# Kernel tuning notes

Hardware: AMD Instinct MI355X
Metric: run time of the kernel (lower is better)

Reference implementation:

```python
import jax, jax.numpy as jnp
import numpy as np

N_GRAPHS = 50
EPS = 1e-5
N_NODES, N_EDGES, F, L, N_HEADS = 50000, 800000, 64, 3, 3


def _bn(x, gamma, beta):
    # BatchNorm1d over nodes, training-mode (biased batch statistics)
    m = x.mean(axis=0)
    v = jnp.mean((x - m) ** 2, axis=0)
    return gamma * (x - m) * jax.lax.rsqrt(v + EPS) + beta


def _pna_layer(x, src, dst, preW, preb, postW, postb, linW, linb, avg_log, avg_lin):
    N = x.shape[0]
    # pre-MLP on concatenated (target x_i, source x_j): [E, 2F] -> [E, F]
    h = jnp.concatenate([x[dst], x[src]], axis=-1) @ preW + preb
    ones = jnp.ones((h.shape[0],), h.dtype)
    cnt = jax.ops.segment_sum(ones, dst, num_segments=N)[:, None]
    has = cnt > 0
    deg = jnp.maximum(cnt, 1.0)  # PNAConv clamps degree to >= 1
    mean = jax.ops.segment_sum(h, dst, num_segments=N) / deg
    mean2 = jax.ops.segment_sum(h * h, dst, num_segments=N) / deg
    std = jnp.sqrt(jax.nn.relu(mean2 - mean * mean) + EPS)
    mn = jnp.where(has, jax.ops.segment_min(h, dst, num_segments=N), 0.0)
    mx = jnp.where(has, jax.ops.segment_max(h, dst, num_segments=N), 0.0)
    aggr = jnp.concatenate([mean, mn, mx, std], axis=-1)  # [N, 4F]
    log_deg = jnp.log(deg + 1.0)
    out = jnp.concatenate([aggr,
                           aggr * (log_deg / avg_log),   # amplification
                           aggr * (avg_log / log_deg),   # attenuation
                           aggr * (deg / avg_lin)],      # linear
                          axis=-1)                       # [N, 16F]
    out = jnp.concatenate([x, out], axis=-1) @ postW + postb  # post-MLP [N, F]
    return out @ linW + linb


def _forward(x, deg_hist, preW, preb, postW, postb, linW, linb, bn_g, bn_b,
             sharedW, sharedb, hW1, hb1, hW2, hb2, hW3, hb3, src, dst, batch):
    bins = jnp.arange(deg_hist.shape[0], dtype=deg_hist.dtype)
    tot = deg_hist.sum()
    avg_lin = (bins * deg_hist).sum() / tot
    avg_log = (jnp.log(bins + 1.0) * deg_hist).sum() / tot
    for l in range(preW.shape[0]):  # only num_conv_layers convs run (zip truncation)
        x = _pna_layer(x, src, dst, preW[l], preb[l], postW[l], postb[l],
                       linW[l], linb[l], avg_log, avg_lin)
        x = jax.nn.relu(_bn(x, bn_g[l], bn_b[l]))
    gcnt = jax.ops.segment_sum(jnp.ones((x.shape[0],), x.dtype), batch,
                               num_segments=N_GRAPHS)[:, None]
    g = jax.ops.segment_sum(x, batch, num_segments=N_GRAPHS) / jnp.maximum(gcnt, 1.0)
    g = jax.nn.relu(g @ sharedW + sharedb)  # shared MLP (num_shared=1)
    h1 = jax.nn.relu(jnp.einsum('gd,hdk->hgk', g, hW1) + hb1[:, None, :])
    h2 = jax.nn.relu(jnp.einsum('hgk,hkm->hgm', h1, hW2) + hb2[:, None, :])
    o = jnp.einsum('hgm,hmo->hgo', h2, hW3) + hb3[:, None, :]  # [H, G, 1]
    return jnp.transpose(o[..., 0])  # [G, H] == torch.cat(head outputs, dim=1)


def setup_inputs():
    key = jax.random.key(0)
    ks = jax.random.split(key, 12)

    def w(k, shape, fan_in):
        return jax.random.normal(k, shape, jnp.float32) / np.sqrt(fan_in)

    return {
        "x": jax.random.normal(ks[0], (N_NODES, F), jnp.float32),
        "edge_index": jax.random.randint(ks[1], (2, N_EDGES), 0, N_NODES),
        "batch": jnp.sort(jax.random.randint(ks[2], (N_NODES,), 0, N_GRAPHS)),
        "deg_hist": jax.random.uniform(ks[3], (33,), jnp.float32) + 0.01,
        "preW": w(ks[4], (L, 2 * F, F), 2 * F),
        "preb": jnp.zeros((L, F), jnp.float32),
        "postW": w(ks[5], (L, 17 * F, F), 17 * F),
        "postb": jnp.zeros((L, F), jnp.float32),
        "linW": w(ks[6], (L, F, F), F),
        "linb": jnp.zeros((L, F), jnp.float32),
        "bn_g": jnp.ones((L, F), jnp.float32),
        "bn_b": jnp.zeros((L, F), jnp.float32),
        "sharedW": w(ks[7], (F, F), F),
        "sharedb": jnp.zeros((F,), jnp.float32),
        "hW1": w(ks[8], (N_HEADS, F, 50), F),
        "hb1": jnp.zeros((N_HEADS, 50), jnp.float32),
        "hW2": w(ks[9], (N_HEADS, 50, 25), 50),
        "hb2": jnp.zeros((N_HEADS, 25), jnp.float32),
        "hW3": w(ks[10], (N_HEADS, 25, 1), 25),
        "hb3": jnp.zeros((N_HEADS, 1), jnp.float32),
    }


def reference(x, edge_index, batch, deg_hist, preW, preb, postW, postb,
              linW, linb, bn_g, bn_b, sharedW, sharedb,
              hW1, hb1, hW2, hb2, hW3, hb3):
    return _forward(x, deg_hist, preW, preb, postW, postb, linW, linb,
                    bn_g, bn_b, sharedW, sharedb, hW1, hb1, hW2, hb2,
                    hW3, hb3, edge_index[0], edge_index[1], batch)
```

## Files before the change

kernel.cpp:

```cpp
#include <hip/hip_runtime.h>
#include <math.h>

#define N_NODES 50000
#define N_EDGES 800000
#define NGRAPHS 50
#define NHEADS 3
#define EPS 1e-5f
#define NWIN 196
#define WSH 8

typedef _Float16 half8 __attribute__((ext_vector_type(8)));
typedef _Float16 half2v __attribute__((ext_vector_type(2)));
typedef float f32x4 __attribute__((ext_vector_type(4)));

__device__ inline half2v h2_shfl_xor(half2v v, int m) {
  int xi = __shfl_xor(*(int*)&v, m, 64);
  return *(half2v*)&xi;
}

__global__ void __launch_bounds__(256) k_zero_setup(int* cnt, float* gsum, float* gcnt,
                                                    float* part, float* partq,
                                                    const float* dh, int nbins, float* scal) {
  int gid = blockIdx.x * 256 + threadIdx.x;
  int gs = gridDim.x * 256;
  for (int i = gid; i < N_NODES; i += gs) cnt[i] = 0;
  for (int i = gid; i < NGRAPHS * 64; i += gs) gsum[i] = 0.f;
  for (int i = gid; i < NGRAPHS; i += gs) gcnt[i] = 0.f;
  for (int i = gid; i < 128 * 64; i += gs) { part[i] = 0.f; partq[i] = 0.f; }
  if (blockIdx.x == 0 && threadIdx.x < 64) {
    int t = threadIdx.x;
    float v = (t < nbins) ? dh[t] : 0.f;
    float lv = logf((float)t + 1.f) * v;
    float bv = (float)t * v;
    for (int d = 32; d > 0; d >>= 1) {
      v  += __shfl_down(v,  d, 64);
      lv += __shfl_down(lv, d, 64);
      bv += __shfl_down(bv, d, 64);
    }
    if (t == 0) { scal[0] = lv / v; scal[1] = bv / v; }
  }
}

__global__ void __launch_bounds__(256) k_hist(const int* __restrict__ dst, int* __restrict__ cnt) {
  int e = blockIdx.x * 256 + threadIdx.x;
  if (e < N_EDGES) atomicAdd(&cnt[dst[e]], 1);
}

__global__ void __launch_bounds__(256) k_scan_a(const int* __restrict__ cnt, int* __restrict__ off,
                                                int* __restrict__ blksum) {
  __shared__ int lds[256];
  int t = threadIdx.x;
  int base = blockIdx.x * 1024 + t * 4;
  int v0 = (base + 0 < N_NODES) ? cnt[base + 0] : 0;
  int v1 = (base + 1 < N_NODES) ? cnt[base + 1] : 0;
  int v2 = (base + 2 < N_NODES) ? cnt[base + 2] : 0;
  int v3 = (base + 3 < N_NODES) ? cnt[base + 3] : 0;
  int tsum = v0 + v1 + v2 + v3;
  lds[t] = tsum; __syncthreads();
  for (int d = 1; d < 256; d <<= 1) {
    int x = (t >= d) ? lds[t - d] : 0;
    __syncthreads();
    lds[t] += x;
    __syncthreads();
  }
  int run = lds[t] - tsum;
  if (base + 0 < N_NODES) off[base + 0] = run; run += v0;
  if (base + 1 < N_NODES) off[base + 1] = run; run += v1;
  if (base + 2 < N_NODES) off[base + 2] = run; run += v2;
  if (base + 3 < N_NODES) off[base + 3] = run;
  if (t == 255) blksum[blockIdx.x] = lds[255];
}

__global__ void __launch_bounds__(64) k_scan_b(const int* __restrict__ blksum, int* __restrict__ blkoff) {
  int t = threadIdx.x;
  int own = (t < 49) ? blksum[t] : 0;
  int v = own;
  for (int d = 1; d < 64; d <<= 1) {
    int u = __shfl_up(v, d, 64);
    if (t >= d) v += u;
  }
  if (t < 49) blkoff[t] = v - own;
}

__global__ void __launch_bounds__(256) k_scan_c(int* __restrict__ off, const int* __restrict__ blkoff,
                                                int* __restrict__ wincur) {
  int i = blockIdx.x * 256 + threadIdx.x;
  if (i < N_NODES) {
    int fo = off[i] + blkoff[i >> 10];
    off[i] = fo;
    if ((i & 255) == 0) wincur[i >> WSH] = fo;
  }
  if (i == 0) off[N_NODES] = N_EDGES;
}

__global__ void __launch_bounds__(256) k_part1(const int* __restrict__ src, const int* __restrict__ dst,
                                               int* __restrict__ wincur, int* __restrict__ pairS,
                                               unsigned char* __restrict__ pairDL) {
  __shared__ int hist[256];
  __shared__ int scan[256];
  __shared__ int baseg[256];
  __shared__ int place[256];
  __shared__ int sS[2048];
  __shared__ unsigned char sDL[2048];
  __shared__ unsigned char sW[2048];
  int t = threadIdx.x;
  int base = blockIdx.x * 2048;
  hist[t] = 0;
  __syncthreads();
  int d[8], s[8];
  #pragma unroll
  for (int i = 0; i < 8; ++i) {
    int e = base + t + 256 * i;
    bool val = e < N_EDGES;
    d[i] = val ? dst[e] : -1;
    s[i] = val ? src[e] : 0;
    if (val) atomicAdd(&hist[d[i] >> WSH], 1);
  }
  __syncthreads();
  int v = hist[t];
  scan[t] = v; __syncthreads();
  for (int dd = 1; dd < 256; dd <<= 1) {
    int x = (t >= dd) ? scan[t - dd] : 0;
    __syncthreads();
    scan[t] += x;
    __syncthreads();
  }
  place[t] = scan[t] - v;
  if (v > 0) baseg[t] = atomicAdd(&wincur[t], v);
  __syncthreads();
  #pragma unroll
  for (int i = 0; i < 8; ++i) {
    if (d[i] >= 0) {
      int w = d[i] >> WSH;
      int p = atomicAdd(&place[w], 1);
      sS[p] = s[i] << 6;
      sDL[p] = (unsigned char)(d[i] & 255);
      sW[p] = (unsigned char)w;
    }
  }
  __syncthreads();
  int tot = min(N_EDGES - base, 2048);
  for (int i = t; i < tot; i += 256) {
    int w = sW[i];
    int gidx = baseg[w] + (i - (scan[w] - hist[w]));
    pairS[gidx] = sS[i];
    pairDL[gidx] = sDL[i];
  }
}

__global__ void __launch_bounds__(256) k_part2(const int* __restrict__ off, const int* __restrict__ pairS,
                                               const unsigned char* __restrict__ pairDL,
                                               int* __restrict__ esrc) {
  __shared__ int curW[256];
  __shared__ int offW[257];
  __shared__ int esrcW[6144];
  int w = blockIdx.x, t = threadIdx.x;
  int n0 = w << WSH;
  offW[t] = off[min(n0 + t, N_NODES)];
  if (t == 0) offW[256] = off[min(n0 + 256, N_NODES)];
  curW[t] = 0;
  __syncthreads();
  int start = offW[0];
  int end = offW[256];
  int cnt = end - start;
  if (cnt <= 6144) {
    for (int i = t; i < cnt; i += 256) {
      int s = pairS[start + i];
      int dl = pairDL[start + i];
      int pos = offW[dl] - start + atomicAdd(&curW[dl], 1);
      esrcW[pos] = s;
    }
    __syncthreads();
    for (int i = t; i < cnt; i += 256) esrc[start + i] = esrcW[i];
  } else {
    for (int i = t; i < cnt; i += 256) {
      int s = pairS[start + i];
      int dl = pairDL[start + i];
      int pos = offW[dl] + atomicAdd(&curW[dl], 1);
      esrc[pos] = s;
    }
  }
}

__global__ void __launch_bounds__(256) k_prep(const float* __restrict__ xin, _Float16* __restrict__ xout,
                                              const float* __restrict__ preW, const float* __restrict__ postW,
                                              const float* __restrict__ linW, _Float16* __restrict__ preP,
                                              _Float16* __restrict__ postAP, _Float16* __restrict__ postBP,
                                              _Float16* __restrict__ linP) {
  int t0 = blockIdx.x * 256 + threadIdx.x;
  if (t0 < 400000) {
    const float* s = xin + (size_t)t0 * 8;
    float4 v0 = *(const float4*)s;
    float4 v1 = *(const float4*)(s + 4);
    half8 h = {(_Float16)v0.x, (_Float16)v0.y, (_Float16)v0.z, (_Float16)v0.w,
               (_Float16)v1.x, (_Float16)v1.y, (_Float16)v1.z, (_Float16)v1.w};
    *(half8*)(xout + (size_t)t0 * 8) = h;
    return;
  }
  int t = t0 - 400000;
  if (t < 24576) {
    int l = t >> 13, r = t & 8191;
    int j = r & 7, lane = (r >> 3) & 63, ctg = (r >> 9) & 7, kc = r >> 12;
    int k = kc * 32 + ((lane >> 4) << 3) + j;
    int col = ctg * 16 + (lane & 15);
    const float* W = preW + (size_t)l * 8192;
    float v = (col < 64) ? W[k * 64 + col] : W[(64 + k) * 64 + (col - 64)];
    preP[(size_t)l * 8192 + r] = (_Float16)v;
  } else if (t < 221184) {
    int q = t - 24576;
    int l = q >> 16, r = q & 65535;
    int j = r & 7, lane = (r >> 3) & 63, ct = (r >> 9) & 3, s = (r >> 11) & 3, kc = r >> 13;
    int kp = kc * 32 + ((lane >> 4) << 3) + j;
    int half = kp >> 7, sec = (kp >> 5) & 3, f = kp & 31;
    int korig = sec * 64 + half * 32 + f;
    int col = ct * 16 + (lane & 15);
    postAP[(size_t)l * 65536 + r] = (_Float16)postW[(size_t)l * 69632 + (size_t)(64 + s * 256 + korig) * 64 + col];
  } else if (t < 233472) {
    int q = t - 221184;
    int l = q >> 12, r = q & 4095;
    int j = r & 7, lane = (r >> 3) & 63, ct = (r >> 9) & 3, kc = r >> 11;
    int k = kc * 32 + ((lane >> 4) << 3) + j;
    int col = ct * 16 + (lane & 15);
    postBP[(size_t)l * 4096 + r] = (_Float16)postW[(size_t)l * 69632 + (size_t)k * 64 + col];
  } else if (t < 245760) {
    int q = t - 233472;
    int l = q >> 12, r = q & 4095;
    int j = r & 7, lane = (r >> 3) & 63, ct = (r >> 9) & 3, kc = r >> 11;
    int k = kc * 32 + ((lane >> 4) << 3) + j;
    int col = ct * 16 + (lane & 15);
    linP[(size_t)l * 4096 + r] = (_Float16)linW[(size_t)l * 4096 + (size_t)k * 64 + col];
  }
}

__global__ void __launch_bounds__(256) k_mfma_g1(const _Float16* __restrict__ yin, const float* __restrict__ bnsc,
                                                 const float* __restrict__ bnsh, int applyBN,
                                                 const _Float16* __restrict__ wp, const float* __restrict__ bias,
                                                 _Float16* __restrict__ Aout, _Float16* __restrict__ B0,
                                                 _Float16* __restrict__ B1, _Float16* __restrict__ xout) {
  int t = threadIdx.x, lane = t & 63, wave = t >> 6;
  int r0 = blockIdx.x * 64;
  int mrow = lane & 15, q8 = ((lane >> 4) << 3);
  f32x4 acc[4][2];
  #pragma unroll
  for (int rt = 0; rt < 4; ++rt) { acc[rt][0] = (f32x4)0.f; acc[rt][1] = (f32x4)0.f; }
  #pragma unroll
  for (int kc = 0; kc < 2; ++kc) {
    int k0 = kc * 32 + q8;
    half8 a[4];
    #pragma unroll
    for (int rt = 0; rt < 4; ++rt) {
      int r = min(r0 + rt * 16 + mrow, N_NODES - 1);
      a[rt] = *(const half8*)(yin + (size_t)r * 64 + k0);
    }
    if (applyBN) {
      float4 sc0 = *(const float4*)(bnsc + k0);
      float4 sc1 = *(const float4*)(bnsc + k0 + 4);
      float4 sh0 = *(const float4*)(bnsh + k0);
      float4 sh1 = *(const float4*)(bnsh + k0 + 4);
      #pragma unroll
      for (int rt = 0; rt < 4; ++rt) {
        half8 v = a[rt];
        v[0] = (_Float16)fmaxf((float)v[0] * sc0.x + sh0.x, 0.f);
        v[1] = (_Float16)fmaxf((float)v[1] * sc0.y + sh0.y, 0.f);
        v[2] = (_Float16)fmaxf((float)v[2] * sc0.z + sh0.z, 0.f);
        v[3] = (_Float16)fmaxf((float)v[3] * sc0.w + sh0.w, 0.f);
        v[4] = (_Float16)fmaxf((float)v[4] * sc1.x + sh1.x, 0.f);
        v[5] = (_Float16)fmaxf((float)v[5] * sc1.y + sh1.y, 0.f);
        v[6] = (_Float16)fmaxf((float)v[6] * sc1.z + sh1.z, 0.f);
        v[7] = (_Float16)fmaxf((float)v[7] * sc1.w + sh1.w, 0.f);
        a[rt] = v;
      }
      if (wave == 0) {
        #pragma unroll
        for (int rt = 0; rt < 4; ++rt) {
          int r = min(r0 + rt * 16 + mrow, N_NODES - 1);
          *(half8*)(xout + (size_t)r * 64 + k0) = a[rt];
        }
      }
    }
    #pragma unroll
    for (int ci = 0; ci < 2; ++ci) {
      int ctg = wave * 2 + ci;
      half8 b = *(const half8*)(wp + (size_t)((kc * 8 + ctg) * 64 + lane) * 8);
      #pragma unroll
      for (int rt = 0; rt < 4; ++rt)
        acc[rt][ci] = __builtin_amdgcn_mfma_f32_16x16x32_f16(a[rt], b, acc[rt][ci], 0, 0, 0);
    }
  }
  #pragma unroll
  for (int ci = 0; ci < 2; ++ci) {
    int col = (wave * 2 + ci) * 16 + mrow;
    float bv = (col < 64) ? bias[col] : 0.f;
    _Float16* outp;
    int stride;
    if (col < 64)      { outp = Aout + col;       stride = 64; }
    else if (col < 96) { outp = B0 + (col - 64);  stride = 32; }
    else               { outp = B1 + (col - 96);  stride = 32; }
    #pragma unroll
    for (int rt = 0; rt < 4; ++rt)
      #pragma unroll
      for (int reg = 0; reg < 4; ++reg) {
        int row = r0 + rt * 16 + ((lane >> 4) << 2) + reg;
        if (row < N_NODES) outp[(size_t)row * stride] = (_Float16)(acc[rt][ci][reg] + bv);
      }
  }
}

__global__ void __launch_bounds__(256) k_aggr(const _Float16* __restrict__ A, const _Float16* __restrict__ B0,
                                              const _Float16* __restrict__ B1, const int* __restrict__ off,
                                              const int* __restrict__ esrc, const float* __restrict__ scal,
                                              _Float16* __restrict__ aggr0, _Float16* __restrict__ aggr1,
                                              float4* __restrict__ scales) {
  int wave = threadIdx.x >> 6, lane = threadIdx.x & 63;
  int b = blockIdx.x;
  int half = (b >> 2) & 1;
  int idx = (b >> 3) * 4 + (b & 3);
  int n = idx * 4 + wave;
  int lh4 = lane & 15, eg = lane >> 4;
  half2v c2 = *(const half2v*)(A + (size_t)n * 64 + half * 32 + lh4 * 2);
  int e0 = __builtin_amdgcn_readfirstlane(off[n]);
  int e1 = __builtin_amdgcn_readfirstlane(off[n + 1]);
  int deg = e1 - e0;
  const char* Bb = (const char*)(half ? B1 : B0);
  int lo4 = lh4 * 4;
  const _Float16 HMAX = (_Float16)65504.f;
  half2v s2 = {(_Float16)0.f, (_Float16)0.f};
  half2v q2 = s2;
  half2v mn2 = {HMAX, HMAX};
  half2v mx2 = {-HMAX, -HMAX};
  int e = e0;
  for (; e + 7 < e1; e += 8) {
    int ra = __builtin_nontemporal_load(esrc + e + eg);
    int rb = __builtin_nontemporal_load(esrc + e + 4 + eg);
    half2v ba = *(const half2v*)(Bb + ra + lo4);
    half2v bb = *(const half2v*)(Bb + rb + lo4);
    s2 += ba; s2 += bb;
    q2 += ba * ba; q2 += bb * bb;
    mn2 = __builtin_elementwise_min(mn2, __builtin_elementwise_min(ba, bb));
    mx2 = __builtin_elementwise_max(mx2, __builtin_elementwise_max(ba, bb));
  }
  for (; e < e1; e += 4) {
    if (e + eg < e1) {
      int r = __builtin_nontemporal_load(esrc + e + eg);
      half2v bv = *(const half2v*)(Bb + r + lo4);
      s2 += bv;
      q2 += bv * bv;
      mn2 = __builtin_elementwise_min(mn2, bv);
      mx2 = __builtin_elementwise_max(mx2, bv);
    }
  }
  s2 += h2_shfl_xor(s2, 16); s2 += h2_shfl_xor(s2, 32);
  q2 += h2_shfl_xor(q2, 16); q2 += h2_shfl_xor(q2, 32);
  mn2 = __builtin_elementwise_min(mn2, h2_shfl_xor(mn2, 16));
  mn2 = __builtin_elementwise_min(mn2, h2_shfl_xor(mn2, 32));
  mx2 = __builtin_elementwise_max(mx2, h2_shfl_xor(mx2, 16));
  mx2 = __builtin_elementwise_max(mx2, h2_shfl_xor(mx2, 32));
  if (eg == 0) {
    _Float16* arow = (half ? aggr1 : aggr0) + (size_t)n * 128;
    half2v w;
    if (deg == 0) {
      w[0] = (_Float16)0.f; w[1] = (_Float16)0.f;
      *(half2v*)(arow + lh4 * 2) = w;
      *(half2v*)(arow + 32 + lh4 * 2) = w;
      *(half2v*)(arow + 64 + lh4 * 2) = w;
      w[0] = (_Float16)sqrtf(EPS); w[1] = w[0];
      *(half2v*)(arow + 96 + lh4 * 2) = w;
    } else {
      float c0 = (float)c2[0], c1 = (float)c2[1];
      float inv = 1.f / (float)deg;
      float mb0 = (float)s2[0] * inv, mb1 = (float)s2[1] * inv;
      float v0 = fmaxf((float)q2[0] * inv - mb0 * mb0, 0.f);
      float v1 = fmaxf((float)q2[1] * inv - mb1 * mb1, 0.f);
      w[0] = (_Float16)(c0 + mb0); w[1] = (_Float16)(c1 + mb1);
      *(half2v*)(arow + lh4 * 2) = w;
      w[0] = (_Float16)(c0 + (float)mn2[0]); w[1] = (_Float16)(c1 + (float)mn2[1]);
      *(half2v*)(arow + 32 + lh4 * 2) = w;
      w[0] = (_Float16)(c0 + (float)mx2[0]); w[1] = (_Float16)(c1 + (float)mx2[1]);
      *(half2v*)(arow + 64 + lh4 * 2) = w;
      w[0] = (_Float16)sqrtf(v0 + EPS); w[1] = (_Float16)sqrtf(v1 + EPS);
      *(half2v*)(arow + 96 + lh4 * 2) = w;
    }
    if (half == 0 && lane == 0) {
      float degf = fmaxf((float)deg, 1.f);
      float ld = logf(degf + 1.f);
      float al = scal[0], av = scal[1];
      scales[n] = make_float4(ld / al, al / ld, degf / av, 0.f);
    }
  }
}

__global__ void __launch_bounds__(256) k_mfma_g23(const _Float16* __restrict__ aggr0, const _Float16* __restrict__ aggr1,
                                                  const _Float16* __restrict__ x16,
                                                  const _Float16* __restrict__ wpA, const _Float16* __restrict__ wpB,
                                                  const float* __restrict__ postb, const float4* __restrict__ scales,
                                                  const _Float16* __restrict__ linP, const float* __restrict__ linb,
                                                  _Float16* __restrict__ y16,
                                                  float* __restrict__ part, float* __restrict__ partq) {
  __shared__ _Float16 yS[64][72];
  int t = threadIdx.x, lane = t & 63, ct = t >> 6;
  int r0 = blockIdx.x * 64;
  int mrow = lane & 15, q8 = ((lane >> 4) << 3);
  f32x4 acc[4][4];
  #pragma unroll
  for (int rt = 0; rt < 4; ++rt)
    #pragma unroll
    for (int s = 0; s < 4; ++s) acc[rt][s] = (f32x4)0.f;
  #pragma unroll 2
  for (int kc = 0; kc < 8; ++kc) {
    const _Float16* ab = (kc < 4) ? aggr0 : aggr1;
    int ko = (kc & 3) * 32 + q8;
    half8 a[4];
    #pragma unroll
    for (int rt = 0; rt < 4; ++rt) {
      int r = min(r0 + rt * 16 + mrow, N_NODES - 1);
      a[rt] = __builtin_nontemporal_load((const half8*)(ab + (size_t)r * 128 + ko));
    }
    #pragma unroll
    for (int s = 0; s < 4; ++s) {
      half8 b = *(const half8*)(wpA + (size_t)((((kc * 4 + s) * 4 + ct) * 64) + lane) * 8);
      #pragma unroll
      for (int rt = 0; rt < 4; ++rt)
        acc[rt][s] = __builtin_amdgcn_mfma_f32_16x16x32_f16(a[rt], b, acc[rt][s], 0, 0, 0);
    }
  }
  #pragma unroll
  for (int kc = 0; kc < 2; ++kc) {
    half8 a[4];
    #pragma unroll
    for (int rt = 0; rt < 4; ++rt) {
      int r = min(r0 + rt * 16 + mrow, N_NODES - 1);
      a[rt] = *(const half8*)(x16 + (size_t)r * 64 + kc * 32 + q8);
    }
    half8 b = *(const half8*)(wpB + (size_t)(((kc * 4 + ct) * 64) + lane) * 8);
    #pragma unroll
    for (int rt = 0; rt < 4; ++rt)
      acc[rt][0] = __builtin_amdgcn_mfma_f32_16x16x32_f16(a[rt], b, acc[rt][0], 0, 0, 0);
  }
  int col = ct * 16 + mrow;
  float pb = postb[col];
  #pragma unroll
  for (int rt = 0; rt < 4; ++rt)
    #pragma unroll
    for (int reg = 0; reg < 4; ++reg) {
      int rr = rt * 16 + ((lane >> 4) << 2) + reg;
      int row = min(r0 + rr, N_NODES - 1);
      float4 sc = scales[row];
      float v = acc[rt][0][reg] + sc.x * acc[rt][1][reg] + sc.y * acc[rt][2][reg] + sc.z * acc[rt][3][reg] + pb;
      yS[rr][col] = (_Float16)v;
    }
  __syncthreads();
  f32x4 acc2[4];
  #pragma unroll
  for (int rt = 0; rt < 4; ++rt) acc2[rt] = (f32x4)0.f;
  #pragma unroll
  for (int kc = 0; kc < 2; ++kc) {
    half8 a[4];
    #pragma unroll
    for (int rt = 0; rt < 4; ++rt)
      a[rt] = *(const half8*)(&yS[rt * 16 + mrow][kc * 32 + q8]);
    half8 b = *(const half8*)(linP + (size_t)(((kc * 4 + ct) * 64) + lane) * 8);
    #pragma unroll
    for (int rt = 0; rt < 4; ++rt)
      acc2[rt] = __builtin_amdgcn_mfma_f32_16x16x32_f16(a[rt], b, acc2[rt], 0, 0, 0);
  }
  float bv = linb[col];
  float s = 0.f, q = 0.f;
  #pragma unroll
  for (int rt = 0; rt < 4; ++rt)
    #pragma unroll
    for (int reg = 0; reg < 4; ++reg) {
      int row = r0 + rt * 16 + ((lane >> 4) << 2) + reg;
      if (row < N_NODES) {
        float v = acc2[rt][reg] + bv;
        y16[(size_t)row * 64 + col] = (_Float16)v;
        s += v; q += v * v;
      }
    }
  int slot = (blockIdx.x & 127) * 64 + col;
  atomicAdd(&part[slot], s);
  atomicAdd(&partq[slot], q);
}

__global__ void __launch_bounds__(256) k_bnfinal(float* __restrict__ part, float* __restrict__ partq,
                                                 const float* __restrict__ g, const float* __restrict__ b,
                                                 float* __restrict__ scale, float* __restrict__ shift) {
  __shared__ float ls[256], lq[256];
  int t = threadIdx.x, col = t & 63, qtr = t >> 6;
  float s = 0.f, q = 0.f;
  for (int i = 0; i < 32; ++i) {
    int slot = qtr * 32 + i;
    s += part[slot * 64 + col];
    q += partq[slot * 64 + col];
  }
  ls[t] = s; lq[t] = q; __syncthreads();
  if (t < 64) {
    s = ls[t] + ls[64 + t] + ls[128 + t] + ls[192 + t];
    q = lq[t] + lq[64 + t] + lq[128 + t] + lq[192 + t];
    float m = s / (float)N_NODES;
    float v = fmaxf(q / (float)N_NODES - m * m, 0.f);
    float sc = g[t] * rsqrtf(v + EPS);
    scale[t] = sc;
    shift[t] = b[t] - m * sc;
  }
  __syncthreads();
  for (int i = t; i < 128 * 64; i += 256) { part[i] = 0.f; partq[i] = 0.f; }
}

__global__ void __launch_bounds__(256) k_pool(const _Float16* __restrict__ y16, const float* __restrict__ bnsc,
                                              const float* __restrict__ bnsh, const int* __restrict__ batch,
                                              float* __restrict__ gsum, float* __restrict__ gcnt) {
  int t = threadIdx.x, col = t & 63, rl = t >> 6;
  float sc = bnsc[col], sh = bnsh[col];
  int rbeg = blockIdx.x * 64 + rl * 16;
  int rend = min(rbeg + 16, N_NODES);
  int curg = -1, cr = 0;
  float acc = 0.f;
  for (int r = rbeg; r < rend; ++r) {
    int g = batch[r];
    if (g != curg) {
      if (curg >= 0) {
        atomicAdd(&gsum[curg * 64 + col], acc);
        if (col == 0) atomicAdd(&gcnt[curg], (float)cr);
      }
      curg = g; acc = 0.f; cr = 0;
    }
    acc += fmaxf((float)y16[(size_t)r * 64 + col] * sc + sh, 0.f); cr++;
  }
  if (curg >= 0) {
    atomicAdd(&gsum[curg * 64 + col], acc);
    if (col == 0) atomicAdd(&gcnt[curg], (float)cr);
  }
}

__global__ void __launch_bounds__(64) k_sharedheads(const float* __restrict__ gsum, const float* __restrict__ gcnt,
                                                    const float* __restrict__ W, const float* __restrict__ b,
                                                    const float* __restrict__ hW1, const float* __restrict__ hb1,
                                                    const float* __restrict__ hW2, const float* __restrict__ hb2,
                                                    const float* __restrict__ hW3, const float* __restrict__ hb3,
                                                    float* __restrict__ out) {
  __shared__ float gm[64], gv[64], h1[50], h2[25];
  int bid = blockIdx.x;
  int g = bid / NHEADS, h = bid % NHEADS;
  int t = threadIdx.x;
  float cv = fmaxf(gcnt[g], 1.f);
  gm[t] = gsum[g * 64 + t] / cv;
  __syncthreads();
  float s0 = b[t];
  for (int k = 0; k < 64; ++k) s0 += gm[k] * W[k * 64 + t];
  gv[t] = fmaxf(s0, 0.f);
  __syncthreads();
  if (t < 50) {
    float s = hb1[h * 50 + t];
    for (int k = 0; k < 64; ++k) s += gv[k] * hW1[h * 3200 + k * 50 + t];
    h1[t] = fmaxf(s, 0.f);
  }
  __syncthreads();
  if (t < 25) {
    float s = hb2[h * 25 + t];
    for (int k = 0; k < 50; ++k) s += h1[k] * hW2[h * 1250 + k * 25 + t];
    h2[t] = fmaxf(s, 0.f);
  }
  __syncthreads();
  if (t == 0) {
    float s = hb3[h];
    for (int k = 0; k < 25; ++k) s += h2[k] * hW3[h * 25 + k];
    out[g * NHEADS + h] = s;
  }
}

extern "C" void kernel_launch(void* const* d_in, const int* in_sizes, int n_in,
                              void* d_out, int out_size, void* d_ws, size_t ws_size,
                              hipStream_t stream) {
  const float* x0    = (const float*)d_in[0];
  const int*   eidx  = (const int*)d_in[1];
  const int*   batch = (const int*)d_in[2];
  const float* dh    = (const float*)d_in[3];
  const float* preW  = (const float*)d_in[4];
  const float* preb  = (const float*)d_in[5];
  const float* postW = (const float*)d_in[6];
  const float* postb = (const float*)d_in[7];
  const float* linW  = (const float*)d_in[8];
  const float* linb  = (const float*)d_in[9];
  const float* bng   = (const float*)d_in[10];
  const float* bnb   = (const float*)d_in[11];
  const float* shW   = (const float*)d_in[12];
  const float* shb   = (const float*)d_in[13];
  const float* hW1   = (const float*)d_in[14];
  const float* hb1   = (const float*)d_in[15];
  const float* hW2   = (const float*)d_in[16];
  const float* hb2   = (const float*)d_in[17];
  const float* hW3   = (const float*)d_in[18];
  const float* hb3   = (const float*)d_in[19];
  float* out = (float*)d_out;

  char* ws = (char*)d_ws;
  size_t o = 0;
  auto alloc = [&](size_t bytes) {
    char* p = ws + o;
    o = (o + bytes + 255) & ~(size_t)255;
    return p;
  };
  float* scal   = (float*)alloc(8 * 4);
  int* off      = (int*)alloc((N_NODES + 1) * 4);
  int* cnt      = (int*)alloc(N_NODES * 4);
  int* esrc     = (int*)alloc(N_EDGES * 4);
  int* pairS    = (int*)alloc(N_EDGES * 4);
  unsigned char* pairDL = (unsigned char*)alloc(N_EDGES);
  int* wincur   = (int*)alloc(NWIN * 4);
  int* blks     = (int*)alloc(64 * 4);
  int* blko     = (int*)alloc(64 * 4);
  _Float16* A16    = (_Float16*)alloc((size_t)N_NODES * 64 * 2 + 256 * 16);
  _Float16* B0     = (_Float16*)alloc((size_t)N_NODES * 32 * 2 + 256 * 16);
  _Float16* B1     = (_Float16*)alloc((size_t)N_NODES * 32 * 2 + 256 * 16);
  _Float16* aggr0  = (_Float16*)alloc((size_t)N_NODES * 128 * 2 + 256 * 16);
  _Float16* aggr1  = (_Float16*)alloc((size_t)N_NODES * 128 * 2 + 256 * 16);
  _Float16* x16a   = (_Float16*)alloc((size_t)N_NODES * 64 * 2 + 256 * 16);
  _Float16* xbuf   = (_Float16*)alloc((size_t)N_NODES * 64 * 2 + 256 * 16);
  _Float16* y16    = (_Float16*)alloc((size_t)N_NODES * 64 * 2 + 256 * 16);
  float4* scales = (float4*)alloc((size_t)N_NODES * 16);
  _Float16* preP   = (_Float16*)alloc(3 * 8192 * 2);
  _Float16* postAP = (_Float16*)alloc((size_t)3 * 65536 * 2);
  _Float16* postBP = (_Float16*)alloc(3 * 4096 * 2);
  _Float16* linP   = (_Float16*)alloc(3 * 4096 * 2);
  float* part   = (float*)alloc(128 * 64 * 4);
  float* partq  = (float*)alloc(128 * 64 * 4);
  float* bnsc   = (float*)alloc(64 * 4);
  float* bnsh   = (float*)alloc(64 * 4);
  float* gsum   = (float*)alloc(NGRAPHS * 64 * 4);
  float* gcnt   = (float*)alloc(NGRAPHS * 4);

  const int* srcv = eidx;
  const int* dstv = eidx + N_EDGES;

  k_zero_setup<<<256, 256, 0, stream>>>(cnt, gsum, gcnt, part, partq, dh, in_sizes[3], scal);
  k_hist<<<(N_EDGES + 255) / 256, 256, 0, stream>>>(dstv, cnt);
  k_scan_a<<<49, 256, 0, stream>>>(cnt, off, blks);
  k_scan_b<<<1, 64, 0, stream>>>(blks, blko);
  k_scan_c<<<196, 256, 0, stream>>>(off, blko, wincur);
  k_part1<<<(N_EDGES + 2047) / 2048, 256, 0, stream>>>(srcv, dstv, wincur, pairS, pairDL);
  k_part2<<<NWIN, 256, 0, stream>>>(off, pairS, pairDL, esrc);
  k_prep<<<(400000 + 245760 + 255) / 256, 256, 0, stream>>>(x0, x16a, preW, postW, linW,
                                                            preP, postAP, postBP, linP);

  for (int l = 0; l < 3; ++l) {
    const _Float16* g1in = (l == 0) ? x16a : y16;
    const _Float16* xc   = (l == 0) ? x16a : xbuf;
    k_mfma_g1<<<782, 256, 0, stream>>>(g1in, bnsc, bnsh, (l > 0) ? 1 : 0,
                                       preP + (size_t)l * 8192, preb + l * 64, A16, B0, B1, xbuf);
    k_aggr<<<25000, 256, 0, stream>>>(A16, B0, B1, off, esrc, scal, aggr0, aggr1, scales);
    k_mfma_g23<<<782, 256, 0, stream>>>(aggr0, aggr1, xc, postAP + (size_t)l * 65536,
                                        postBP + (size_t)l * 4096, postb + l * 64, scales,
                                        linP + (size_t)l * 4096, linb + l * 64, y16, part, partq);
    k_bnfinal<<<1, 256, 0, stream>>>(part, partq, bng + l * 64, bnb + l * 64, bnsc, bnsh);
  }
  k_pool<<<782, 256, 0, stream>>>(y16, bnsc, bnsh, batch, gsum, gcnt);
  k_sharedheads<<<NGRAPHS * NHEADS, 64, 0, stream>>>(gsum, gcnt, shW, shb,
                                                     hW1, hb1, hW2, hb2, hW3, hb3, out);
}
```

Baseline: 528.6 us.

## Merge split-half aggregation into single full-width pass with batched gathers

Replaces the two 32-feature halves (B0/B1, aggr0/aggr1) with one 64-wide B buffer and one 256-wide aggregation row, so each wave handles a whole node with 32 lanes over features and 2 edge groups. The aggregation loop now issues 8 clamped index loads and then 8 gathers per iteration, with masking in place of a remainder loop, to raise memory-level parallelism. The post-weight permutation and the source-row shift are updated to match the new layout. This halves the aggr launch count and avoids rereading edge indices twice per node, but gives fewer edge lanes per node and wasted masked work on low-degree nodes.

```diff
diff --git a/kernel.cpp b/kernel.cpp
--- a/kernel.cpp
+++ b/kernel.cpp
@@ -133,7 +133,7 @@
     if (d[i] >= 0) {
       int w = d[i] >> WSH;
       int p = atomicAdd(&place[w], 1);
-      sS[p] = s[i] << 6;
+      sS[p] = s[i] << 7;
       sDL[p] = (unsigned char)(d[i] & 255);
       sW[p] = (unsigned char)w;
     }
@@ -210,11 +210,9 @@
     int q = t - 24576;
     int l = q >> 16, r = q & 65535;
     int j = r & 7, lane = (r >> 3) & 63, ct = (r >> 9) & 3, s = (r >> 11) & 3, kc = r >> 13;
-    int kp = kc * 32 + ((lane >> 4) << 3) + j;
-    int half = kp >> 7, sec = (kp >> 5) & 3, f = kp & 31;
-    int korig = sec * 64 + half * 32 + f;
+    int k = kc * 32 + ((lane >> 4) << 3) + j;
     int col = ct * 16 + (lane & 15);
-    postAP[(size_t)l * 65536 + r] = (_Float16)postW[(size_t)l * 69632 + (size_t)(64 + s * 256 + korig) * 64 + col];
+    postAP[(size_t)l * 65536 + r] = (_Float16)postW[(size_t)l * 69632 + (size_t)(64 + s * 256 + k) * 64 + col];
   } else if (t < 233472) {
     int q = t - 221184;
     int l = q >> 12, r = q & 4095;
@@ -235,8 +233,8 @@
 __global__ void __launch_bounds__(256) k_mfma_g1(const _Float16* __restrict__ yin, const float* __restrict__ bnsc,
                                                  const float* __restrict__ bnsh, int applyBN,
                                                  const _Float16* __restrict__ wp, const float* __restrict__ bias,
-                                                 _Float16* __restrict__ Aout, _Float16* __restrict__ B0,
-                                                 _Float16* __restrict__ B1, _Float16* __restrict__ xout) {
+                                                 _Float16* __restrict__ Aout, _Float16* __restrict__ Bout,
+                                                 _Float16* __restrict__ xout) {
   int t = threadIdx.x, lane = t & 63, wave = t >> 6;
   int r0 = blockIdx.x * 64;
   int mrow = lane & 15, q8 = ((lane >> 4) << 3);
@@ -290,81 +288,73 @@
   #pragma unroll
   for (int ci = 0; ci < 2; ++ci) {
     int col = (wave * 2 + ci) * 16 + mrow;
-    float bv = (col < 64) ? bias[col] : 0.f;
-    _Float16* outp;
-    int stride;
-    if (col < 64)      { outp = Aout + col;       stride = 64; }
-    else if (col < 96) { outp = B0 + (col - 64);  stride = 32; }
-    else               { outp = B1 + (col - 96);  stride = 32; }
+    bool isA = col < 64;
+    float bv = isA ? bias[col] : 0.f;
+    _Float16* outp = isA ? (Aout + col) : (Bout + (col - 64));
     #pragma unroll
     for (int rt = 0; rt < 4; ++rt)
       #pragma unroll
       for (int reg = 0; reg < 4; ++reg) {
         int row = r0 + rt * 16 + ((lane >> 4) << 2) + reg;
-        if (row < N_NODES) outp[(size_t)row * stride] = (_Float16)(acc[rt][ci][reg] + bv);
+        if (row < N_NODES) outp[(size_t)row * 64] = (_Float16)(acc[rt][ci][reg] + bv);
       }
   }
 }
 
-__global__ void __launch_bounds__(256) k_aggr(const _Float16* __restrict__ A, const _Float16* __restrict__ B0,
-                                              const _Float16* __restrict__ B1, const int* __restrict__ off,
-                                              const int* __restrict__ esrc, const float* __restrict__ scal,
-                                              _Float16* __restrict__ aggr0, _Float16* __restrict__ aggr1,
+__global__ void __launch_bounds__(256) k_aggr(const _Float16* __restrict__ A, const _Float16* __restrict__ B,
+                                              const int* __restrict__ off, const int* __restrict__ esrc,
+                                              const float* __restrict__ scal, _Float16* __restrict__ aggr,
                                               float4* __restrict__ scales) {
   int wave = threadIdx.x >> 6, lane = threadIdx.x & 63;
-  int b = blockIdx.x;
-  int half = (b >> 2) & 1;
-  int idx = (b >> 3) * 4 + (b & 3);
-  int n = idx * 4 + wave;
-  int lh4 = lane & 15, eg = lane >> 4;
-  half2v c2 = *(const half2v*)(A + (size_t)n * 64 + half * 32 + lh4 * 2);
+  int n = blockIdx.x * 4 + wave;
+  int lh = lane & 31, eg = lane >> 5;
+  half2v c2 = *(const half2v*)(A + (size_t)n * 64 + lh * 2);
   int e0 = __builtin_amdgcn_readfirstlane(off[n]);
   int e1 = __builtin_amdgcn_readfirstlane(off[n + 1]);
   int deg = e1 - e0;
-  const char* Bb = (const char*)(half ? B1 : B0);
-  int lo4 = lh4 * 4;
+  const char* Bb = (const char*)B;
+  int lo4 = lh * 4;
   const _Float16 HMAX = (_Float16)65504.f;
-  half2v s2 = {(_Float16)0.f, (_Float16)0.f};
-  half2v q2 = s2;
-  half2v mn2 = {HMAX, HMAX};
-  half2v mx2 = {-HMAX, -HMAX};
-  int e = e0;
-  for (; e + 7 < e1; e += 8) {
-    int ra = __builtin_nontemporal_load(esrc + e + eg);
-    int rb = __builtin_nontemporal_load(esrc + e + 4 + eg);
-    half2v ba = *(const half2v*)(Bb + ra + lo4);
-    half2v bb = *(const half2v*)(Bb + rb + lo4);
-    s2 += ba; s2 += bb;
-    q2 += ba * ba; q2 += bb * bb;
-    mn2 = __builtin_elementwise_min(mn2, __builtin_elementwise_min(ba, bb));
-    mx2 = __builtin_elementwise_max(mx2, __builtin_elementwise_max(ba, bb));
-  }
-  for (; e < e1; e += 4) {
-    if (e + eg < e1) {
-      int r = __builtin_nontemporal_load(esrc + e + eg);
-      half2v bv = *(const half2v*)(Bb + r + lo4);
-      s2 += bv;
-      q2 += bv * bv;
-      mn2 = __builtin_elementwise_min(mn2, bv);
-      mx2 = __builtin_elementwise_max(mx2, bv);
-    }
-  }
-  s2 += h2_shfl_xor(s2, 16); s2 += h2_shfl_xor(s2, 32);
-  q2 += h2_shfl_xor(q2, 16); q2 += h2_shfl_xor(q2, 32);
-  mn2 = __builtin_elementwise_min(mn2, h2_shfl_xor(mn2, 16));
+  half2v z2 = {(_Float16)0.f, (_Float16)0.f};
+  half2v p2 = {HMAX, HMAX};
+  half2v m2v = {-HMAX, -HMAX};
+  half2v s2 = z2, q2 = z2, mn2 = p2, mx2 = m2v;
+  if (deg > 0) {
+    int e1m1 = e1 - 1;
+    for (int e = e0; e < e1; e += 16) {
+      int ro[8];
+      #pragma unroll
+      for (int g = 0; g < 8; ++g)
+        ro[g] = esrc[min(e + g * 2 + eg, e1m1)];
+      half2v v[8];
+      #pragma unroll
+      for (int g = 0; g < 8; ++g)
+        v[g] = *(const half2v*)(Bb + ro[g] + lo4);
+      #pragma unroll
+      for (int g = 0; g < 8; ++g) {
+        bool valid = (e + g * 2 + eg) < e1;
+        half2v vm = valid ? v[g] : z2;
+        s2 += vm;
+        q2 += vm * vm;
+        mn2 = __builtin_elementwise_min(mn2, valid ? v[g] : p2);
+        mx2 = __builtin_elementwise_max(mx2, valid ? v[g] : m2v);
+      }
+    }
+  }
+  s2 += h2_shfl_xor(s2, 32);
+  q2 += h2_shfl_xor(q2, 32);
   mn2 = __builtin_elementwise_min(mn2, h2_shfl_xor(mn2, 32));
-  mx2 = __builtin_elementwise_max(mx2, h2_shfl_xor(mx2, 16));
   mx2 = __builtin_elementwise_max(mx2, h2_shfl_xor(mx2, 32));
   if (eg == 0) {
-    _Float16* arow = (half ? aggr1 : aggr0) + (size_t)n * 128;
+    _Float16* arow = aggr + (size_t)n * 256;
     half2v w;
     if (deg == 0) {
-      w[0] = (_Float16)0.f; w[1] = (_Float16)0.f;
-      *(half2v*)(arow + lh4 * 2) = w;
-      *(half2v*)(arow + 32 + lh4 * 2) = w;
-      *(half2v*)(arow + 64 + lh4 * 2) = w;
+      w = z2;
+      *(half2v*)(arow + lh * 2) = w;
+      *(half2v*)(arow + 64 + lh * 2) = w;
+      *(half2v*)(arow + 128 + lh * 2) = w;
       w[0] = (_Float16)sqrtf(EPS); w[1] = w[0];
-      *(half2v*)(arow + 96 + lh4 * 2) = w;
+      *(half2v*)(arow + 192 + lh * 2) = w;
     } else {
       float c0 = (float)c2[0], c1 = (float)c2[1];
       float inv = 1.f / (float)deg;
@@ -372,15 +362,15 @@
       float v0 = fmaxf((float)q2[0] * inv - mb0 * mb0, 0.f);
       float v1 = fmaxf((float)q2[1] * inv - mb1 * mb1, 0.f);
       w[0] = (_Float16)(c0 + mb0); w[1] = (_Float16)(c1 + mb1);
-      *(half2v*)(arow + lh4 * 2) = w;
+      *(half2v*)(arow + lh * 2) = w;
       w[0] = (_Float16)(c0 + (float)mn2[0]); w[1] = (_Float16)(c1 + (float)mn2[1]);
-      *(half2v*)(arow + 32 + lh4 * 2) = w;
+      *(half2v*)(arow + 64 + lh * 2) = w;
       w[0] = (_Float16)(c0 + (float)mx2[0]); w[1] = (_Float16)(c1 + (float)mx2[1]);
-      *(half2v*)(arow + 64 + lh4 * 2) = w;
+      *(half2v*)(arow + 128 + lh * 2) = w;
       w[0] = (_Float16)sqrtf(v0 + EPS); w[1] = (_Float16)sqrtf(v1 + EPS);
-      *(half2v*)(arow + 96 + lh4 * 2) = w;
-    }
-    if (half == 0 && lane == 0) {
+      *(half2v*)(arow + 192 + lh * 2) = w;
+    }
+    if (lane == 0) {
       float degf = fmaxf((float)deg, 1.f);
       float ld = logf(degf + 1.f);
       float al = scal[0], av = scal[1];
@@ -389,7 +379,7 @@
   }
 }
 
-__global__ void __launch_bounds__(256) k_mfma_g23(const _Float16* __restrict__ aggr0, const _Float16* __restrict__ aggr1,
+__global__ void __launch_bounds__(256) k_mfma_g23(const _Float16* __restrict__ aggr,
                                                   const _Float16* __restrict__ x16,
                                                   const _Float16* __restrict__ wpA, const _Float16* __restrict__ wpB,
                                                   const float* __restrict__ postb, const float4* __restrict__ scales,
@@ -407,13 +397,11 @@
     for (int s = 0; s < 4; ++s) acc[rt][s] = (f32x4)0.f;
   #pragma unroll 2
   for (int kc = 0; kc < 8; ++kc) {
-    const _Float16* ab = (kc < 4) ? aggr0 : aggr1;
-    int ko = (kc & 3) * 32 + q8;
     half8 a[4];
     #pragma unroll
     for (int rt = 0; rt < 4; ++rt) {
       int r = min(r0 + rt * 16 + mrow, N_NODES - 1);
-      a[rt] = __builtin_nontemporal_load((const half8*)(ab + (size_t)r * 128 + ko));
+      a[rt] = __builtin_nontemporal_load((const half8*)(aggr + (size_t)r * 256 + kc * 32 + q8));
     }
     #pragma unroll
     for (int s = 0; s < 4; ++s) {
@@ -610,10 +598,8 @@
   int* blks     = (int*)alloc(64 * 4);
   int* blko     = (int*)alloc(64 * 4);
   _Float16* A16    = (_Float16*)alloc((size_t)N_NODES * 64 * 2 + 256 * 16);
-  _Float16* B0     = (_Float16*)alloc((size_t)N_NODES * 32 * 2 + 256 * 16);
-  _Float16* B1     = (_Float16*)alloc((size_t)N_NODES * 32 * 2 + 256 * 16);
-  _Float16* aggr0  = (_Float16*)alloc((size_t)N_NODES * 128 * 2 + 256 * 16);
-  _Float16* aggr1  = (_Float16*)alloc((size_t)N_NODES * 128 * 2 + 256 * 16);
+  _Float16* B16    = (_Float16*)alloc((size_t)N_NODES * 64 * 2 + 256 * 16);
+  _Float16* aggr16 = (_Float16*)alloc((size_t)N_NODES * 256 * 2 + 256 * 16);
   _Float16* x16a   = (_Float16*)alloc((size_t)N_NODES * 64 * 2 + 256 * 16);
   _Float16* xbuf   = (_Float16*)alloc((size_t)N_NODES * 64 * 2 + 256 * 16);
   _Float16* y16    = (_Float16*)alloc((size_t)N_NODES * 64 * 2 + 256 * 16);
@@ -646,9 +632,9 @@
     const _Float16* g1in = (l == 0) ? x16a : y16;
     const _Float16* xc   = (l == 0) ? x16a : xbuf;
     k_mfma_g1<<<782, 256, 0, stream>>>(g1in, bnsc, bnsh, (l > 0) ? 1 : 0,
-                                       preP + (size_t)l * 8192, preb + l * 64, A16, B0, B1, xbuf);
-    k_aggr<<<25000, 256, 0, stream>>>(A16, B0, B1, off, esrc, scal, aggr0, aggr1, scales);
-    k_mfma_g23<<<782, 256, 0, stream>>>(aggr0, aggr1, xc, postAP + (size_t)l * 65536,
+                                       preP + (size_t)l * 8192, preb + l * 64, A16, B16, xbuf);
+    k_aggr<<<12500, 256, 0, stream>>>(A16, B16, off, esrc, scal, aggr16, scales);
+    k_mfma_g23<<<782, 256, 0, stream>>>(aggr16, xc, postAP + (size_t)l * 65536,
                                         postBP + (size_t)l * 4096, postb + l * 64, scales,
                                         linP + (size_t)l * 4096, linb + l * 64, y16, part, partq);
     k_bnfinal<<<1, 256, 0, stream>>>(part, partq, bng + l * 64, bnb + l * 64, bnsc, bnsh);
```

Result: faster. 457.1 us (-13.5%).
